# Kernel optimization log

Hardware: AMD Instinct MI355X
Metric: run time of the kernel (lower is better)

Reference implementation:

```python
import jax, jax.numpy as jnp
import numpy as np

N_EMBD = 1024
N_HEAD = 16
D_HEAD = N_EMBD // N_HEAD


def setup_inputs() -> dict:
    key = jax.random.key(0)
    ks = jax.random.split(key, 5)
    x = jax.random.normal(ks[0], (4, 2048, N_EMBD), dtype=jnp.float32)
    s = 1.0 / np.sqrt(N_EMBD)
    Wq = jax.random.normal(ks[1], (N_EMBD, N_EMBD), dtype=jnp.float32) * s
    Wk = jax.random.normal(ks[2], (N_EMBD, N_EMBD), dtype=jnp.float32) * s
    Wv = jax.random.normal(ks[3], (N_EMBD, N_EMBD), dtype=jnp.float32) * s
    Wo = jax.random.normal(ks[4], (N_EMBD, N_EMBD), dtype=jnp.float32) * s
    return {"x": x, "Wq": Wq, "Wk": Wk, "Wv": Wv, "Wo": Wo}


def reference(x, Wq, Wk, Wv, Wo):
    B, S, E = x.shape
    H, Dh = N_HEAD, D_HEAD
    scale = 1.0 / np.sqrt(Dh)  # LayerwiseSDPA(d_head) -> scale by 1/sqrt(d_head)

    def proj(W):
        # nn.Linear(no bias): y = x @ W.T ; reshape to [B,H,S,Dh]
        return (x @ W.T).reshape(B, S, H, Dh).transpose(0, 2, 1, 3)

    q, k, v = proj(Wq), proj(Wk), proj(Wv)
    scores = jnp.einsum('bhsd,bhtd->bhst', q, k) * scale  # [B,H,S,S]
    causal = jnp.tril(jnp.ones((S, S), dtype=bool))
    scores = jnp.where(causal, scores, jnp.finfo(scores.dtype).min)
    attn = jax.nn.softmax(scores, axis=-1)
    y = jnp.einsum('bhst,bhtd->bhsd', attn, v)  # [B,H,S,Dh]
    y = y.transpose(0, 2, 1, 3).reshape(B, S, E)
    return y @ Wo.T
```

## Files before the change

### kernel.cpp

```cpp
#include <hip/hip_runtime.h>

typedef __bf16 bf16;
typedef bf16  bf16x8 __attribute__((ext_vector_type(8)));
typedef bf16  bf16x4 __attribute__((ext_vector_type(4)));
typedef short s16x4  __attribute__((ext_vector_type(4)));
typedef float f32x4  __attribute__((ext_vector_type(4)));

#define AS1 __attribute__((address_space(1)))
#define AS3 __attribute__((address_space(3)))

#define SQLEN 2048
#define EMB   1024

__global__ __launch_bounds__(256) void cvt_f32_bf16(const float* __restrict__ in,
                                                    bf16* __restrict__ out, int n8) {
  int i = blockIdx.x * blockDim.x + threadIdx.x;
  if (i >= n8) return;
  const float4* p = (const float4*)in + (size_t)i * 2;
  float4 a = p[0], b = p[1];
  bf16x8 o;
  o[0] = (bf16)a.x; o[1] = (bf16)a.y; o[2] = (bf16)a.z; o[3] = (bf16)a.w;
  o[4] = (bf16)b.x; o[5] = (bf16)b.y; o[6] = (bf16)b.z; o[7] = (bf16)b.w;
  *((bf16x8*)out + i) = o;
}

__global__ __launch_bounds__(256) void cvt_w4(const float* __restrict__ w0, const float* __restrict__ w1,
                                              const float* __restrict__ w2, const float* __restrict__ w3,
                                              bf16* o0, bf16* o1, bf16* o2, bf16* o3, int n8) {
  const float* in; bf16* out;
  switch (blockIdx.y) {
    case 0: in = w0; out = o0; break;
    case 1: in = w1; out = o1; break;
    case 2: in = w2; out = o2; break;
    default: in = w3; out = o3; break;
  }
  int i = blockIdx.x * blockDim.x + threadIdx.x;
  if (i >= n8) return;
  const float4* p = (const float4*)in + (size_t)i * 2;
  float4 a = p[0], b = p[1];
  bf16x8 o;
  o[0] = (bf16)a.x; o[1] = (bf16)a.y; o[2] = (bf16)a.z; o[3] = (bf16)a.w;
  o[4] = (bf16)b.x; o[5] = (bf16)b.y; o[6] = (bf16)b.z; o[7] = (bf16)b.w;
  *((bf16x8*)out + i) = o;
}

__device__ __forceinline__
void gemm_body_f32(const bf16* __restrict__ A, const bf16* __restrict__ B,
                   float* __restrict__ Cf, int M, int N, int K,
                   bf16* Asl, bf16* Bsl) {
  const int tid  = threadIdx.x;
  const int lane = tid & 63, wave = tid >> 6;
  const int quad = lane >> 4, col = lane & 15;
  const int m0 = blockIdx.x * 128, n0 = blockIdx.y * 128;
  const int wr = wave >> 1, wc = wave & 1;

  f32x4 acc[4][4];
  const f32x4 fz = {0.f, 0.f, 0.f, 0.f};
#pragma unroll
  for (int i = 0; i < 4; ++i)
#pragma unroll
    for (int j = 0; j < 4; ++j) acc[i][j] = fz;

  const int srow = lane >> 2;
  const int sk   = lane & 3;

  auto stage = [&](int buf, int k0) {
#pragma unroll
    for (int r = 0; r < 2; ++r) {
      const int c      = wave * 2 + r;
      const int row    = c * 16 + srow;
      const int gchunk = sk ^ (row & 3);
      const bf16* ga = A + (size_t)(m0 + row) * K + k0 + gchunk * 8;
      const bf16* gb = B + (size_t)(n0 + row) * K + k0 + gchunk * 8;
      __builtin_amdgcn_global_load_lds((const AS1 void*)ga, (AS3 void*)(Asl + buf * 4096 + c * 512), 16, 0, 0);
      __builtin_amdgcn_global_load_lds((const AS1 void*)gb, (AS3 void*)(Bsl + buf * 4096 + c * 512), 16, 0, 0);
    }
  };

  const int nk = K >> 5;
  stage(0, 0);
  for (int it = 0; it < nk; ++it) {
    __syncthreads();
    if (it + 1 < nk) stage((it + 1) & 1, (it + 1) << 5);
    const bf16* As = Asl + (it & 1) * 4096;
    const bf16* Bs = Bsl + (it & 1) * 4096;

    bf16x8 af[4], bfr[4];
#pragma unroll
    for (int i = 0; i < 4; ++i) {
      const int r = wr * 64 + i * 16 + col;
      af[i] = *(const bf16x8*)&As[r * 32 + ((quad ^ (col & 3)) * 8)];
    }
#pragma unroll
    for (int j = 0; j < 4; ++j) {
      const int r = wc * 64 + j * 16 + col;
      bfr[j] = *(const bf16x8*)&Bs[r * 32 + ((quad ^ (col & 3)) * 8)];
    }
#pragma unroll
    for (int i = 0; i < 4; ++i)
#pragma unroll
      for (int j = 0; j < 4; ++j)
        acc[i][j] = __builtin_amdgcn_mfma_f32_16x16x32_bf16(af[i], bfr[j], acc[i][j], 0, 0, 0);
  }

#pragma unroll
  for (int i = 0; i < 4; ++i) {
#pragma unroll
    for (int j = 0; j < 4; ++j) {
      const int gm0 = m0 + wr * 64 + i * 16 + quad * 4;
      const int gn  = n0 + wc * 64 + j * 16 + col;
#pragma unroll
      for (int r = 0; r < 4; ++r)
        Cf[(size_t)(gm0 + r) * N + gn] = acc[i][j][r];
    }
  }
}

__global__ __launch_bounds__(256, 2)
void gemm_qkv(const bf16* __restrict__ A, const bf16* __restrict__ Wq,
              const bf16* __restrict__ Wk, const bf16* __restrict__ Wv,
              bf16* __restrict__ Qo, bf16* __restrict__ Ko, bf16* __restrict__ Vto,
              float qscale) {
  __shared__ bf16 Asl[2 * 4096];
  __shared__ bf16 Bsl[3][2 * 4096];

  const int tid  = threadIdx.x;
  const int lane = tid & 63, wave = tid >> 6;
  const int quad = lane >> 4, col = lane & 15;
  const int m0 = blockIdx.x * 128, n0 = blockIdx.y * 128;
  const int wr = wave >> 1, wc = wave & 1;
  const int K = 1024, N = 1024;

  const bf16* const Bp[3] = {Wq, Wk, Wv};

  f32x4 acc[3][4][4];
  const f32x4 fz = {0.f, 0.f, 0.f, 0.f};
#pragma unroll
  for (int s = 0; s < 3; ++s)
#pragma unroll
    for (int i = 0; i < 4; ++i)
#pragma unroll
      for (int j = 0; j < 4; ++j) acc[s][i][j] = fz;

  const int srow = lane >> 2;
  const int sk   = lane & 3;

  auto stage = [&](int buf, int k0) {
#pragma unroll
    for (int r = 0; r < 2; ++r) {
      const int c      = wave * 2 + r;
      const int row    = c * 16 + srow;
      const int gchunk = sk ^ (row & 3);
      const bf16* ga = A + (size_t)(m0 + row) * K + k0 + gchunk * 8;
      __builtin_amdgcn_global_load_lds((const AS1 void*)ga,
          (AS3 void*)(Asl + buf * 4096 + c * 512), 16, 0, 0);
#pragma unroll
      for (int s = 0; s < 3; ++s) {
        const bf16* gb = Bp[s] + (size_t)(n0 + row) * K + k0 + gchunk * 8;
        __builtin_amdgcn_global_load_lds((const AS1 void*)gb,
            (AS3 void*)(&Bsl[s][buf * 4096 + c * 512]), 16, 0, 0);
      }
    }
  };

  const int nk = K >> 5;
  stage(0, 0);
  for (int it = 0; it < nk; ++it) {
    __syncthreads();
    if (it + 1 < nk) stage((it + 1) & 1, (it + 1) << 5);
    const bf16* As = Asl + (it & 1) * 4096;

    bf16x8 af[4];
#pragma unroll
    for (int i = 0; i < 4; ++i) {
      const int r = wr * 64 + i * 16 + col;
      af[i] = *(const bf16x8*)&As[r * 32 + ((quad ^ (col & 3)) * 8)];
    }
#pragma unroll
    for (int s = 0; s < 3; ++s) {
      const bf16* Bs = &Bsl[s][(it & 1) * 4096];
      bf16x8 bfr[4];
#pragma unroll
      for (int j = 0; j < 4; ++j) {
        const int r = wc * 64 + j * 16 + col;
        bfr[j] = *(const bf16x8*)&Bs[r * 32 + ((quad ^ (col & 3)) * 8)];
      }
#pragma unroll
      for (int i = 0; i < 4; ++i)
#pragma unroll
        for (int j = 0; j < 4; ++j)
          acc[s][i][j] = __builtin_amdgcn_mfma_f32_16x16x32_bf16(af[i], bfr[j], acc[s][i][j], 0, 0, 0);
    }
  }

#pragma unroll
  for (int s = 0; s < 3; ++s) {
    const float sc = (s == 0) ? qscale : 1.0f;
#pragma unroll
    for (int i = 0; i < 4; ++i) {
#pragma unroll
      for (int j = 0; j < 4; ++j) {
        const int gm0 = m0 + wr * 64 + i * 16 + quad * 4;
        const int gn  = n0 + wc * 64 + j * 16 + col;
        if (s == 2) {
          bf16x4 ob;
#pragma unroll
          for (int r = 0; r < 4; ++r) ob[r] = (bf16)(acc[s][i][j][r]);
          const int bb = gm0 >> 11;
          const int t_ = gm0 & 2047;
          *(bf16x4*)&Vto[((size_t)(bb * 1024 + gn)) * 2048 + t_] = ob;
        } else {
          bf16* C = (s == 0) ? Qo : Ko;
#pragma unroll
          for (int r = 0; r < 4; ++r)
            C[(size_t)(gm0 + r) * N + gn] = (bf16)(acc[s][i][j][r] * sc);
        }
      }
    }
  }
}

__global__ __launch_bounds__(256, 2)
void gemm_o(const bf16* __restrict__ A, const bf16* __restrict__ W, float* __restrict__ C) {
  __shared__ bf16 Asl[2 * 4096];
  __shared__ bf16 Bsl[2 * 4096];
  gemm_body_f32(A, W, C, 8192, 1024, 1024, Asl, Bsl);
}

__global__ __launch_bounds__(512, 4)
void attn_flash(const bf16* __restrict__ Q, const bf16* __restrict__ K,
                const bf16* __restrict__ Vt, bf16* __restrict__ Y) {
  __shared__ bf16 Ksb0[2 * 8192];
  __shared__ bf16 Vsb0[2 * 8192];

  const int tid  = threadIdx.x;
  const int lane = tid & 63, wave = tid >> 6;
  const int quad = lane >> 4, col = lane & 15;

  const int B_ = blockIdx.x;
  const int bh = (B_ & 7) * 8 + (B_ >> 6);
  const int p  = (B_ >> 3) & 7;
  const int h  = bh & 15;
  const int b  = bh >> 4;
  const int hc = h * 64;
  const size_t rowBase = (size_t)b * SQLEN;

  const int srow8 = lane >> 3;
  const int sch   = lane & 7;
  const int a7    = col & 7;

  auto stageKV = [&](int buf, int t0) {
#pragma unroll
    for (int i = 0; i < 2; ++i) {
      const int krow = wave * 16 + i * 8 + srow8;
      const int kch  = sch ^ srow8;
      const bf16* gk = K + (rowBase + t0 + krow) * EMB + hc + kch * 8;
      __builtin_amdgcn_global_load_lds((const AS1 void*)gk,
          (AS3 void*)(Ksb0 + buf * 8192 + wave * 1024 + i * 512), 16, 0, 0);
      const int vrow = wave * 8 + i * 4 + (lane >> 4);
      const int vch  = (lane & 15) ^ (vrow & 7);
      const bf16* gv = Vt + ((size_t)(b * EMB + hc + vrow)) * SQLEN + t0 + vch * 8;
      __builtin_amdgcn_global_load_lds((const AS1 void*)gv,
          (AS3 void*)(Vsb0 + buf * 8192 + wave * 1024 + i * 512), 16, 0, 0);
    }
  };

  const s16x4 ones = {(short)0x3F80, (short)0x3F80, (short)0x3F80, (short)0x3F80};

  for (int halfIdx = 0; halfIdx < 2; ++halfIdx) {
    const int qt = halfIdx == 0 ? (15 - p) : p;
    const int q0 = qt * 128;
    const int ntt = qt + 1;

    stageKV(0, 0);

    bf16x8 qf0, qf1;
    {
      const int row = wave * 16 + col;
      const bf16* gq = Q + (rowBase + q0 + row) * EMB + hc + quad * 8;
      qf0 = *(const bf16x8*)gq;
      qf1 = *(const bf16x8*)(gq + 32);
    }
    __syncthreads();

    float m_i = -INFINITY;
    f32x4 o[4], ol;
    const f32x4 fz = {0.f, 0.f, 0.f, 0.f};
#pragma unroll
    for (int dd = 0; dd < 4; ++dd) o[dd] = fz;
    ol = fz;

    for (int tt = 0; tt < ntt; ++tt) {
      const int t0 = tt * 128;
      const int cur = tt & 1;
      if (tt + 1 < ntt) stageKV(cur ^ 1, t0 + 128);
      const bf16* Ks = Ksb0 + cur * 8192;
      const bf16* Vs = Vsb0 + cur * 8192;

      f32x4 s[8];
      __builtin_amdgcn_s_setprio(1);
#pragma unroll
      for (int sl = 0; sl < 8; ++sl) {
        const bf16x8 kf0 = *(const bf16x8*)&Ks[(sl * 16 + col) * 64 + ((quad ^ a7) * 8)];
        const bf16x8 kf1 = *(const bf16x8*)&Ks[(sl * 16 + col) * 64 + (((quad ^ 4) ^ a7) * 8)];
        f32x4 z = fz;
        z = __builtin_amdgcn_mfma_f32_16x16x32_bf16(kf0, qf0, z, 0, 0, 0);
        s[sl] = __builtin_amdgcn_mfma_f32_16x16x32_bf16(kf1, qf1, z, 0, 0, 0);
      }
      __builtin_amdgcn_s_setprio(0);

      if (tt == qt) {
        const int qg = q0 + wave * 16 + col;
#pragma unroll
        for (int sl = 0; sl < 8; ++sl)
#pragma unroll
          for (int r = 0; r < 4; ++r)
            if (t0 + sl * 16 + quad * 4 + r > qg) s[sl][r] = -INFINITY;
      }

      bf16x4 pb[8];
      {
        float mx = s[0][0];
#pragma unroll
        for (int sl = 0; sl < 8; ++sl)
#pragma unroll
          for (int r = 0; r < 4; ++r) mx = fmaxf(mx, s[sl][r]);
        mx = fmaxf(mx, __shfl_xor(mx, 16));
        mx = fmaxf(mx, __shfl_xor(mx, 32));
        if (!__all(mx <= m_i + 8.f)) {
          const float mnew = fmaxf(m_i, mx);
          const float a = __builtin_amdgcn_exp2f(m_i - mnew);
#pragma unroll
          for (int dd = 0; dd < 4; ++dd) o[dd] *= a;
          ol *= a;
          m_i = mnew;
        }
#pragma unroll
        for (int sl = 0; sl < 8; ++sl)
#pragma unroll
          for (int r = 0; r < 4; ++r)
            pb[sl][r] = (bf16)__builtin_amdgcn_exp2f(s[sl][r] - m_i);
      }

      __builtin_amdgcn_s_setprio(1);
#pragma unroll
      for (int sl = 0; sl < 8; ++sl) {
        const s16x4 pf = __builtin_bit_cast(s16x4, pb[sl]);
        ol = __builtin_amdgcn_mfma_f32_16x16x16bf16_1k(ones, pf, ol, 0, 0, 0);
        const int cch  = 2 * sl + (quad >> 1);
        const int half = quad & 1;
#pragma unroll
        for (int dd = 0; dd < 4; ++dd) {
          const int row = dd * 16 + col;
          const bf16x4 vb = *(const bf16x4*)&Vs[row * 128 + ((cch ^ a7) * 8) + half * 4];
          const s16x4 vf = __builtin_bit_cast(s16x4, vb);
          o[dd] = __builtin_amdgcn_mfma_f32_16x16x16bf16_1k(vf, pf, o[dd], 0, 0, 0);
        }
      }
      __builtin_amdgcn_s_setprio(0);
      __syncthreads();
    }

    {
      const float rl = __builtin_amdgcn_rcpf(ol[0]);
      const size_t yrow = (rowBase + q0 + wave * 16 + col) * EMB + hc;
#pragma unroll
      for (int dd = 0; dd < 4; ++dd) {
        bf16x4 ob;
#pragma unroll
        for (int r = 0; r < 4; ++r) ob[r] = (bf16)(o[dd][r] * rl);
        *(bf16x4*)&Y[yrow + dd * 16 + quad * 4] = ob;
      }
    }
  }
}

extern "C" void kernel_launch(void* const* d_in, const int* in_sizes, int n_in,
                              void* d_out, int out_size, void* d_ws, size_t ws_size,
                              hipStream_t stream) {
  const float* x  = (const float*)d_in[0];
  const float* Wq = (const float*)d_in[1];
  const float* Wk = (const float*)d_in[2];
  const float* Wv = (const float*)d_in[3];
  const float* Wo = (const float*)d_in[4];
  float* out = (float*)d_out;

  const size_t ME = 8192ull * 1024ull;
  const size_t WE = 1024ull * 1024ull;
  bf16* ws  = (bf16*)d_ws;
  bf16* xb  = ws;
  bf16* wqb = xb + ME;
  bf16* wkb = wqb + WE;
  bf16* wvb = wkb + WE;
  bf16* wob = wvb + WE;
  bf16* Qb  = wob + WE;
  bf16* Kb  = Qb + ME;
  bf16* Vtb = Kb + ME;
  bf16* Yb  = Vtb + ME;

  cvt_f32_bf16<<<(int)(ME / 8 / 256), 256, 0, stream>>>(x, xb, (int)(ME / 8));
  cvt_w4<<<dim3((int)(WE / 8 / 256), 4), 256, 0, stream>>>(Wq, Wk, Wv, Wo, wqb, wkb, wvb, wob, (int)(WE / 8));

  const float qscale = 0.125f * 1.4426950408889634f;
  gemm_qkv<<<dim3(64, 8), 256, 0, stream>>>(xb, wqb, wkb, wvb, Qb, Kb, Vtb, qscale);

  attn_flash<<<512, 512, 0, stream>>>(Qb, Kb, Vtb, Yb);

  gemm_o<<<dim3(64, 8), 256, 0, stream>>>(Yb, wob, out);
}
```

Before: 240.5 us.

## Process two 16-row query groups per wave in flash attention, halving block size

```diff
diff --git a/kernel.cpp b/kernel.cpp
--- a/kernel.cpp
+++ b/kernel.cpp
@@ -227,7 +227,7 @@
   gemm_body_f32(A, W, C, 8192, 1024, 1024, Asl, Bsl);
 }
 
-__global__ __launch_bounds__(512, 4)
+__global__ __launch_bounds__(256, 2)
 void attn_flash(const bf16* __restrict__ Q, const bf16* __restrict__ K,
                 const bf16* __restrict__ Vt, bf16* __restrict__ Y) {
   __shared__ bf16 Ksb0[2 * 8192];
@@ -251,17 +251,17 @@
 
   auto stageKV = [&](int buf, int t0) {
 #pragma unroll
-    for (int i = 0; i < 2; ++i) {
-      const int krow = wave * 16 + i * 8 + srow8;
+    for (int i = 0; i < 4; ++i) {
+      const int krow = wave * 32 + i * 8 + srow8;
       const int kch  = sch ^ srow8;
       const bf16* gk = K + (rowBase + t0 + krow) * EMB + hc + kch * 8;
       __builtin_amdgcn_global_load_lds((const AS1 void*)gk,
-          (AS3 void*)(Ksb0 + buf * 8192 + wave * 1024 + i * 512), 16, 0, 0);
-      const int vrow = wave * 8 + i * 4 + (lane >> 4);
+          (AS3 void*)(Ksb0 + buf * 8192 + wave * 2048 + i * 512), 16, 0, 0);
+      const int vrow = wave * 16 + i * 4 + (lane >> 4);
       const int vch  = (lane & 15) ^ (vrow & 7);
       const bf16* gv = Vt + ((size_t)(b * EMB + hc + vrow)) * SQLEN + t0 + vch * 8;
       __builtin_amdgcn_global_load_lds((const AS1 void*)gv,
-          (AS3 void*)(Vsb0 + buf * 8192 + wave * 1024 + i * 512), 16, 0, 0);
+          (AS3 void*)(Vsb0 + buf * 8192 + wave * 2048 + i * 512), 16, 0, 0);
     }
   };
 
@@ -274,21 +274,25 @@
 
     stageKV(0, 0);
 
-    bf16x8 qf0, qf1;
-    {
-      const int row = wave * 16 + col;
+    bf16x8 qf[2][2];
+#pragma unroll
+    for (int g = 0; g < 2; ++g) {
+      const int row = g * 64 + wave * 16 + col;
       const bf16* gq = Q + (rowBase + q0 + row) * EMB + hc + quad * 8;
-      qf0 = *(const bf16x8*)gq;
-      qf1 = *(const bf16x8*)(gq + 32);
+      qf[g][0] = *(const bf16x8*)gq;
+      qf[g][1] = *(const bf16x8*)(gq + 32);
     }
     __syncthreads();
 
-    float m_i = -INFINITY;
-    f32x4 o[4], ol;
+    float m_i[2] = {-INFINITY, -INFINITY};
+    f32x4 o[2][4], ol[2];
     const f32x4 fz = {0.f, 0.f, 0.f, 0.f};
 #pragma unroll
-    for (int dd = 0; dd < 4; ++dd) o[dd] = fz;
-    ol = fz;
+    for (int g = 0; g < 2; ++g) {
+#pragma unroll
+      for (int dd = 0; dd < 4; ++dd) o[g][dd] = fz;
+      ol[g] = fz;
+    }
 
     for (int tt = 0; tt < ntt; ++tt) {
       const int t0 = tt * 128;
@@ -297,56 +301,65 @@
       const bf16* Ks = Ksb0 + cur * 8192;
       const bf16* Vs = Vsb0 + cur * 8192;
 
-      f32x4 s[8];
+      f32x4 s[2][8];
       __builtin_amdgcn_s_setprio(1);
 #pragma unroll
       for (int sl = 0; sl < 8; ++sl) {
         const bf16x8 kf0 = *(const bf16x8*)&Ks[(sl * 16 + col) * 64 + ((quad ^ a7) * 8)];
         const bf16x8 kf1 = *(const bf16x8*)&Ks[(sl * 16 + col) * 64 + (((quad ^ 4) ^ a7) * 8)];
-        f32x4 z = fz;
-        z = __builtin_amdgcn_mfma_f32_16x16x32_bf16(kf0, qf0, z, 0, 0, 0);
-        s[sl] = __builtin_amdgcn_mfma_f32_16x16x32_bf16(kf1, qf1, z, 0, 0, 0);
+#pragma unroll
+        for (int g = 0; g < 2; ++g) {
+          f32x4 z = fz;
+          z = __builtin_amdgcn_mfma_f32_16x16x32_bf16(kf0, qf[g][0], z, 0, 0, 0);
+          s[g][sl] = __builtin_amdgcn_mfma_f32_16x16x32_bf16(kf1, qf[g][1], z, 0, 0, 0);
+        }
       }
       __builtin_amdgcn_s_setprio(0);
 
       if (tt == qt) {
-        const int qg = q0 + wave * 16 + col;
+#pragma unroll
+        for (int g = 0; g < 2; ++g) {
+          const int qg = q0 + g * 64 + wave * 16 + col;
+#pragma unroll
+          for (int sl = 0; sl < 8; ++sl)
+#pragma unroll
+            for (int r = 0; r < 4; ++r)
+              if (t0 + sl * 16 + quad * 4 + r > qg) s[g][sl][r] = -INFINITY;
+        }
+      }
+
+      bf16x4 pb[2][8];
+#pragma unroll
+      for (int g = 0; g < 2; ++g) {
+        float mx = s[g][0][0];
 #pragma unroll
         for (int sl = 0; sl < 8; ++sl)
 #pragma unroll
-          for (int r = 0; r < 4; ++r)
-            if (t0 + sl * 16 + quad * 4 + r > qg) s[sl][r] = -INFINITY;
-      }
-
-      bf16x4 pb[8];
-      {
-        float mx = s[0][0];
-#pragma unroll
-        for (int sl = 0; sl < 8; ++sl)
-#pragma unroll
-          for (int r = 0; r < 4; ++r) mx = fmaxf(mx, s[sl][r]);
+          for (int r = 0; r < 4; ++r) mx = fmaxf(mx, s[g][sl][r]);
         mx = fmaxf(mx, __shfl_xor(mx, 16));
         mx = fmaxf(mx, __shfl_xor(mx, 32));
-        if (!__all(mx <= m_i + 8.f)) {
-          const float mnew = fmaxf(m_i, mx);
-          const float a = __builtin_amdgcn_exp2f(m_i - mnew);
-#pragma unroll
-          for (int dd = 0; dd < 4; ++dd) o[dd] *= a;
-          ol *= a;
-          m_i = mnew;
+        if (!__all(mx <= m_i[g] + 8.f)) {
+          const float mnew = fmaxf(m_i[g], mx);
+          const float a = __builtin_amdgcn_exp2f(m_i[g] - mnew);
+#pragma unroll
+          for (int dd = 0; dd < 4; ++dd) o[g][dd] *= a;
+          ol[g] *= a;
+          m_i[g] = mnew;
         }
 #pragma unroll
         for (int sl = 0; sl < 8; ++sl)
 #pragma unroll
           for (int r = 0; r < 4; ++r)
-            pb[sl][r] = (bf16)__builtin_amdgcn_exp2f(s[sl][r] - m_i);
+            pb[g][sl][r] = (bf16)__builtin_amdgcn_exp2f(s[g][sl][r] - m_i[g]);
       }
 
       __builtin_amdgcn_s_setprio(1);
 #pragma unroll
       for (int sl = 0; sl < 8; ++sl) {
-        const s16x4 pf = __builtin_bit_cast(s16x4, pb[sl]);
-        ol = __builtin_amdgcn_mfma_f32_16x16x16bf16_1k(ones, pf, ol, 0, 0, 0);
+        const s16x4 pf0 = __builtin_bit_cast(s16x4, pb[0][sl]);
+        const s16x4 pf1 = __builtin_bit_cast(s16x4, pb[1][sl]);
+        ol[0] = __builtin_amdgcn_mfma_f32_16x16x16bf16_1k(ones, pf0, ol[0], 0, 0, 0);
+        ol[1] = __builtin_amdgcn_mfma_f32_16x16x16bf16_1k(ones, pf1, ol[1], 0, 0, 0);
         const int cch  = 2 * sl + (quad >> 1);
         const int half = quad & 1;
 #pragma unroll
@@ -354,21 +367,23 @@
           const int row = dd * 16 + col;
           const bf16x4 vb = *(const bf16x4*)&Vs[row * 128 + ((cch ^ a7) * 8) + half * 4];
           const s16x4 vf = __builtin_bit_cast(s16x4, vb);
-          o[dd] = __builtin_amdgcn_mfma_f32_16x16x16bf16_1k(vf, pf, o[dd], 0, 0, 0);
+          o[0][dd] = __builtin_amdgcn_mfma_f32_16x16x16bf16_1k(vf, pf0, o[0][dd], 0, 0, 0);
+          o[1][dd] = __builtin_amdgcn_mfma_f32_16x16x16bf16_1k(vf, pf1, o[1][dd], 0, 0, 0);
         }
       }
       __builtin_amdgcn_s_setprio(0);
       __syncthreads();
     }
 
-    {
-      const float rl = __builtin_amdgcn_rcpf(ol[0]);
-      const size_t yrow = (rowBase + q0 + wave * 16 + col) * EMB + hc;
+#pragma unroll
+    for (int g = 0; g < 2; ++g) {
+      const float rl = __builtin_amdgcn_rcpf(ol[g][0]);
+      const size_t yrow = (rowBase + q0 + g * 64 + wave * 16 + col) * EMB + hc;
 #pragma unroll
       for (int dd = 0; dd < 4; ++dd) {
         bf16x4 ob;
 #pragma unroll
-        for (int r = 0; r < 4; ++r) ob[r] = (bf16)(o[dd][r] * rl);
+        for (int r = 0; r < 4; ++r) ob[r] = (bf16)(o[g][dd][r] * rl);
         *(bf16x4*)&Y[yrow + dd * 16 + quad * 4] = ob;
       }
     }
@@ -404,7 +419,7 @@
   const float qscale = 0.125f * 1.4426950408889634f;
   gemm_qkv<<<dim3(64, 8), 256, 0, stream>>>(xb, wqb, wkb, wvb, Qb, Kb, Vtb, qscale);
 
-  attn_flash<<<512, 512, 0, stream>>>(Qb, Kb, Vtb, Yb);
+  attn_flash<<<512, 256, 0, stream>>>(Qb, Kb, Vtb, Yb);
 
   gemm_o<<<dim3(64, 8), 256, 0, stream>>>(Yb, wob, out);
 }
```

Measured after the change: 243.3 us. No clear change (+1.2%).
